# Kernel tuning notes

Hardware: AMD Instinct MI355X
Metric: run time of the kernel (lower is better)

The kernel has to match this reference:

```python
import jax, jax.numpy as jnp
import numpy as np
from jax.scipy.linalg import solve_triangular

EPS = 1e-5
CHUNK = 64

def _rms(x, w, eps=EPS):
    return x * jax.lax.rsqrt(jnp.mean(x * x, axis=-1, keepdims=True) + eps) * w

def _l2norm(x, eps=1e-6):
    return x * jax.lax.rsqrt(jnp.sum(x * x, axis=-1, keepdims=True) + eps)

def _causal_conv(x, w):
    # x: [B,T,C], w: [C,K] depthwise causal short conv
    K = w.shape[1]
    T = x.shape[1]
    xp = jnp.pad(x, ((0, 0), (K - 1, 0), (0, 0)))
    return sum(xp[:, j:j + T, :] * w[:, j] for j in range(K))

def _chunk_gated_delta_rule(q, k, v, g, beta, chunk=CHUNK):
    # q,k: [B,H,T,Dk] (l2-normalized, q pre-scaled); v: [B,H,T,Dv]; g,beta: [B,H,T]
    Bb, H, T, Dk = k.shape
    Dv = v.shape[-1]
    N = T // chunk
    qc, kc, vc = (a.reshape(Bb, H, N, chunk, -1) for a in (q, k, v))
    gc = g.reshape(Bb, H, N, chunk)
    bc = beta.reshape(Bb, H, N, chunk)
    gcs = jnp.cumsum(gc, axis=-1)  # within-chunk cumulative log-decay
    tri = jnp.tril(jnp.ones((chunk, chunk), bool))
    tri_s = jnp.tril(jnp.ones((chunk, chunk), bool), -1)
    diff = gcs[..., :, None] - gcs[..., None, :]
    decay = jnp.where(tri, jnp.exp(jnp.where(tri, diff, 0.0)), 0.0)  # [B,H,N,C,C]
    k_beta = kc * bc[..., None]
    v_beta = vc * bc[..., None]
    A = jnp.einsum('bhnck,bhndk->bhncd', k_beta, kc) * decay
    A = jnp.where(tri_s, A, 0.0)
    eye = jnp.eye(chunk, dtype=q.dtype)
    Tmat = solve_triangular(eye + A, jnp.broadcast_to(eye, A.shape), lower=True)  # (I+A)^-1
    u = Tmat @ v_beta                               # [B,H,N,C,Dv]
    w = Tmat @ (k_beta * jnp.exp(gcs)[..., None])   # [B,H,N,C,Dk]

    def step(S, inp):
        q_i, k_i, u_i, w_i, g_i, dm_i = inp
        attn = jnp.where(tri, jnp.einsum('bhck,bhdk->bhcd', q_i, k_i) * dm_i, 0.0)
        v_new = u_i - w_i @ S
        o_i = (q_i * jnp.exp(g_i)[..., None]) @ S + attn @ v_new
        g_last = g_i[..., -1]
        k_dec = k_i * jnp.exp(g_last[..., None] - g_i)[..., None]
        S = S * jnp.exp(g_last)[..., None, None] + jnp.einsum('bhck,bhcv->bhkv', k_dec, v_new)
        return S, o_i

    xs = tuple(jnp.moveaxis(a, 2, 0) for a in (qc, kc, u, w, gcs, decay))
    S0 = jnp.zeros((Bb, H, Dk, Dv), q.dtype)
    _, outs = jax.lax.scan(step, S0, xs)  # [N,B,H,C,Dv]
    return jnp.moveaxis(outs, 0, 2).reshape(Bb, H, T, Dv)

def _layer_forward(x, mask, ln1_w, qkvz_w, ba_w, conv_w, A_log, dt_bias,
                   o_norm_w, out_w, ln2_w, gate_w, up_w, down_w):
    B, T, D = x.shape
    H = A_log.shape[0]
    kd = qkvz_w.shape[0] // 4  # key_dim == value_dim here (k_heads==v_heads, Dk==Dv)
    vd = kd
    Dk = kd // H
    Dv = vd // H
    silu = jax.nn.silu
    h = _rms(x, ln1_w)
    qkvz = h @ qkvz_w.T
    q, k, v, z = jnp.split(qkvz, [kd, 2 * kd, 2 * kd + vd], axis=-1)
    b, a = jnp.split(h @ ba_w.T, 2, axis=-1)  # [B,T,H] each
    mixed = jnp.concatenate([q, k, v], axis=-1) * mask[..., None]
    mixed = silu(_causal_conv(mixed, conv_w))
    q, k, v = jnp.split(mixed, [kd, 2 * kd], axis=-1)
    q = _l2norm(q.reshape(B, T, H, Dk))
    k = _l2norm(k.reshape(B, T, H, Dk))
    v = v.reshape(B, T, H, Dv)
    beta = jax.nn.sigmoid(b) * mask[..., None]
    g = -jnp.exp(A_log) * jax.nn.softplus(a + dt_bias) * mask[..., None]
    scale = Dk ** -0.5
    bhtd = lambda t: jnp.transpose(t, (0, 2, 1, 3))
    o = _chunk_gated_delta_rule(bhtd(q) * scale, bhtd(k), bhtd(v),
                                jnp.transpose(g, (0, 2, 1)), jnp.transpose(beta, (0, 2, 1)))
    o = jnp.transpose(o, (0, 2, 1, 3))  # [B,T,H,Dv]
    o = _rms(o, o_norm_w) * silu(z.reshape(B, T, H, Dv))  # gated RMSNorm
    x = x + o.reshape(B, T, vd) @ out_w.T
    h2 = _rms(x, ln2_w)
    mlp_out = (silu(h2 @ gate_w.T) * (h2 @ up_w.T)) @ down_w.T
    return x + mlp_out

def setup_inputs():
    key = jax.random.key(0)
    ks = jax.random.split(key, 12)
    B, T, D, H, Dk, Dv, M, K = 1, 4096, 2048, 16, 128, 128, 8192, 4
    kd, vd = H * Dk, H * Dv
    nrm = lambda i, shp, sc=0.02: jax.random.normal(ks[i], shp, jnp.float32) * sc
    return {
        'x': nrm(0, (B, T, D), 1.0),
        'mask': jnp.ones((B, T), jnp.float32),
        'ln1_w': jnp.ones((D,), jnp.float32),
        'qkvz_w': nrm(1, (2 * kd + 2 * vd, D)),
        'ba_w': nrm(2, (2 * H, D)),
        'conv_w': nrm(3, (2 * kd + vd, K), 0.3),
        'A_log': jnp.log(jax.random.uniform(ks[4], (H,), jnp.float32, 1.0, 16.0)),
        'dt_bias': nrm(5, (H,), 0.5),
        'o_norm_w': jnp.ones((Dv,), jnp.float32),
        'out_w': nrm(6, (D, vd)),
        'ln2_w': jnp.ones((D,), jnp.float32),
        'gate_w': nrm(7, (M, D)),
        'up_w': nrm(8, (M, D)),
        'down_w': nrm(9, (D, M)),
    }

def reference(x, mask, ln1_w, qkvz_w, ba_w, conv_w, A_log, dt_bias,
              o_norm_w, out_w, ln2_w, gate_w, up_w, down_w):
    return _layer_forward(x, mask, ln1_w, qkvz_w, ba_w, conv_w, A_log, dt_bias,
                          o_norm_w, out_w, ln2_w, gate_w, up_w, down_w)
```

## Files before the change

kernel.cpp:

```cpp
#include <hip/hip_runtime.h>
#include <math.h>

#define T_LEN 4096
#define DMODEL 2048
#define NH 16
#define CQKV 6144
#define CQKVZ 8192
#define SCALE 0.08838834764831845f

using bf16x8 = __attribute__((ext_vector_type(8))) short;
using f32x4  = __attribute__((ext_vector_type(4))) float;

__device__ __forceinline__ float siluf(float x) { return x / (1.0f + __expf(-x)); }

__device__ __forceinline__ unsigned short f2bf(float f) {
  unsigned int u = __float_as_uint(f);
  u = (u + 0x7FFFu + ((u >> 16) & 1u)) >> 16;
  return (unsigned short)u;
}
__device__ __forceinline__ float bf2f(unsigned short u) {
  return __uint_as_float(((unsigned int)u) << 16);
}
__device__ __forceinline__ ushort4 pack4(float a, float b, float c, float d) {
  ushort4 r; r.x = f2bf(a); r.y = f2bf(b); r.z = f2bf(c); r.w = f2bf(d); return r;
}

__device__ __forceinline__ void gl_lds16(const unsigned short* g, unsigned short* l) {
  __builtin_amdgcn_global_load_lds(
      (const __attribute__((address_space(1))) void*)g,
      (__attribute__((address_space(3))) void*)l, 16, 0, 0);
}

template<int MODE>
__global__ __launch_bounds__(256) void rmsnorm_kernel(const float* __restrict__ x,
                                                      const float* __restrict__ w,
                                                      float* __restrict__ outf,
                                                      unsigned short* __restrict__ outb) {
  const int t = blockIdx.x;
  const int tid = threadIdx.x;
  const float4* xr = (const float4*)(x + (size_t)t * DMODEL);
  float4 v0 = xr[tid];
  float4 v1 = xr[tid + 256];
  float s = v0.x*v0.x + v0.y*v0.y + v0.z*v0.z + v0.w*v0.w
          + v1.x*v1.x + v1.y*v1.y + v1.z*v1.z + v1.w*v1.w;
#pragma unroll
  for (int off = 32; off > 0; off >>= 1) s += __shfl_down(s, off);
  __shared__ float red[4];
  if ((tid & 63) == 0) red[tid >> 6] = s;
  __syncthreads();
  const float tot = red[0] + red[1] + red[2] + red[3];
  const float r = rsqrtf(tot * (1.0f / DMODEL) + 1e-5f);
  const float4* wr = (const float4*)w;
  const float4 w0 = wr[tid], w1 = wr[tid + 256];
  float4 o0, o1;
  o0.x = v0.x*r*w0.x; o0.y = v0.y*r*w0.y; o0.z = v0.z*r*w0.z; o0.w = v0.w*r*w0.w;
  o1.x = v1.x*r*w1.x; o1.y = v1.y*r*w1.y; o1.z = v1.z*r*w1.z; o1.w = v1.w*r*w1.w;
  if (MODE == 1) {
    float4* orow = (float4*)(outf + (size_t)t * DMODEL);
    orow[tid] = o0;
    orow[tid + 256] = o1;
  }
  ushort4* brow = (ushort4*)(outb + (size_t)t * DMODEL);
  brow[tid] = pack4(o0.x, o0.y, o0.z, o0.w);
  brow[tid + 256] = pack4(o1.x, o1.y, o1.z, o1.w);
}

__global__ __launch_bounds__(256) void f2b_kernel(const float* __restrict__ in,
                                                  unsigned short* __restrict__ out) {
  const size_t i = (size_t)blockIdx.x * 256 + threadIdx.x;
  const float4 a = ((const float4*)in)[2 * i];
  const float4 b = ((const float4*)in)[2 * i + 1];
  ((ushort4*)out)[2 * i] = pack4(a.x, a.y, a.z, a.w);
  ((ushort4*)out)[2 * i + 1] = pack4(b.x, b.y, b.z, b.w);
}

template<int EPI, int BM>
__global__ __launch_bounds__(512, 1) void gemm256_kernel(const unsigned short* __restrict__ A,
                                                         const unsigned short* __restrict__ B,
                                                         float* __restrict__ Cf,
                                                         unsigned short* __restrict__ Cb,
                                                         int M, int N, int K) {
  constexpr int BN = 256;
  constexpr int MI = BM / 32;
  constexpr int AW = BM / 128;
  __shared__ __align__(16) unsigned short lds[3][(BM + BN) * 32];
  const int nbm = M / BM, nbn = N / BN, nwg = nbm * nbn;
  const int nt = K >> 5;
  int bmi, bni;
  {
    const int bid = blockIdx.x;
    const int cpx = nwg >> 3;
    int sc = 1;
    while (sc * sc < cpx) sc <<= 1;
    if (sc * sc > cpx) sc >>= 1;
    const int scn = (sc > 0) ? (cpx / sc) : 0;
    if ((nwg & 7) == 0 && sc > 0 && sc * scn == cpx && (nbm % sc) == 0 && (nbn % scn) == 0) {
      const int chunk = bid & 7, widx = bid >> 3;
      const int regc = nbn / scn;
      bmi = (chunk / regc) * sc + widx / scn;
      bni = (chunk % regc) * scn + widx % scn;
    } else {
      bmi = bid / nbn; bni = bid % nbn;
    }
  }
  const int bm = bmi * BM, bn = bni * BN;
  const int tid = threadIdx.x;
  const int wv = tid >> 6, ln = tid & 63;
  const int fr = ln & 15, qq = ln >> 4;
  const int wm = wv >> 2, wn = wv & 3;
  const int ra0 = wm * (BM / 2), rb0 = wn * 64;
  const int lrow = ln >> 2;
  const int lslot = ln & 3;

  f32x4 acc[MI][4];
  const f32x4 zero = {0.f, 0.f, 0.f, 0.f};
#pragma unroll
  for (int mi = 0; mi < MI; mi++)
#pragma unroll
    for (int ni = 0; ni < 4; ni++) acc[mi][ni] = zero;

  auto stageA = [&](int buf, int t) {
    const int k0 = t << 5;
#pragma unroll
    for (int q = 0; q < AW; q++) {
      const int lr = q * 128 + wv * 16 + lrow;
      const int sl = lslot ^ ((lr >> 1) & 3);
      gl_lds16(A + (size_t)(bm + lr) * K + k0 + sl * 8,
               &lds[buf][(q * 128 + wv * 16) * 32]);
    }
  };
  auto stageB = [&](int buf, int t) {
    const int k0 = t << 5;
#pragma unroll
    for (int q = 0; q < 2; q++) {
      const int lr = q * 128 + wv * 16 + lrow;
      const int sl = lslot ^ ((lr >> 1) & 3);
      gl_lds16(B + (size_t)(bn + lr) * K + k0 + sl * 8,
               &lds[buf][BM * 32 + (q * 128 + wv * 16) * 32]);
    }
  };

  stageA(0, 0); stageB(0, 0);
  stageA(1, 1); stageB(1, 1);
  if constexpr (AW == 2) asm volatile("s_waitcnt vmcnt(4)" ::: "memory");
  else                   asm volatile("s_waitcnt vmcnt(3)" ::: "memory");
  __builtin_amdgcn_s_barrier();
  asm volatile("" ::: "memory");

  for (int t = 0; t < nt; t++) {
    const int cb = t % 3;
    const int b2 = (t + 2) % 3;
    const unsigned short* lA = &lds[cb][0];
    const unsigned short* lB = &lds[cb][BM * 32];
    bf16x8 bfr[4];
#pragma unroll
    for (int ni = 0; ni < 4; ni++) {
      const int r = rb0 + ni * 16 + fr;
      bfr[ni] = *(const bf16x8*)&lB[r * 32 + ((qq ^ ((r >> 1) & 3)) << 3)];
    }
    bf16x8 afr[MI];
#pragma unroll
    for (int mi = 0; mi < MI; mi++) {
      const int r = ra0 + mi * 16 + fr;
      afr[mi] = *(const bf16x8*)&lA[r * 32 + ((qq ^ ((r >> 1) & 3)) << 3)];
    }
    if (t + 2 < nt) { stageA(b2, t + 2); stageB(b2, t + 2); }
    __builtin_amdgcn_s_setprio(1);
#pragma unroll
    for (int mi = 0; mi < MI; mi++)
#pragma unroll
      for (int ni = 0; ni < 4; ni++)
        acc[mi][ni] = __builtin_amdgcn_mfma_f32_16x16x32_bf16(afr[mi], bfr[ni], acc[mi][ni], 0, 0, 0);
    __builtin_amdgcn_s_setprio(0);
    if (t + 1 < nt) {
      asm volatile("s_waitcnt lgkmcnt(0)" ::: "memory");
      if (t + 2 < nt) {
        if constexpr (AW == 2) asm volatile("s_waitcnt vmcnt(4)" ::: "memory");
        else                   asm volatile("s_waitcnt vmcnt(3)" ::: "memory");
      } else {
        asm volatile("s_waitcnt vmcnt(0)" ::: "memory");
      }
      __builtin_amdgcn_s_barrier();
      asm volatile("" ::: "memory");
    }
  }

  const int cm4 = qq * 4;
#pragma unroll
  for (int mi = 0; mi < MI; mi++) {
#pragma unroll
    for (int ni = 0; ni < 4; ni++) {
#pragma unroll
      for (int r = 0; r < 4; r++) {
        const int grow = bm + ra0 + mi * 16 + cm4 + r;
        const int gcol = bn + rb0 + ni * 16 + fr;
        const size_t off = (size_t)grow * N + gcol;
        const float v = acc[mi][ni][r];
        if (EPI == 0) {
          Cb[off] = f2bf(v);
        } else if (EPI == 1) {
          Cf[off] += v;
        } else {
          Cb[off] = f2bf(siluf(bf2f(Cb[off])) * v);
        }
      }
    }
  }
}

__global__ __launch_bounds__(256) void ba_gemm_kernel(const float* __restrict__ h_in,
                                                      const float* __restrict__ ba_w,
                                                      float* __restrict__ ba_out) {
  __shared__ __align__(16) float hl[2048];
  __shared__ float red[32][9];
  const int t = blockIdx.x;
  const int tid = threadIdx.x;
  const float4* hr = (const float4*)(h_in + (size_t)t * DMODEL);
  ((float4*)hl)[tid] = hr[tid];
  ((float4*)hl)[tid + 256] = hr[tid + 256];
  __syncthreads();
  const int c = tid & 31;
  const int p = tid >> 5;
  const float* wrow = ba_w + (size_t)c * DMODEL + p * 256;
  const float* hrow = hl + p * 256;
  float s = 0.f;
#pragma unroll 8
  for (int k = 0; k < 256; k++) s += hrow[k] * wrow[k];
  red[c][p] = s;
  __syncthreads();
  if (tid < 32) {
    float tot = 0.f;
#pragma unroll
    for (int q = 0; q < 8; q++) tot += red[tid][q];
    ba_out[(size_t)t * 32 + tid] = tot;
  }
}

__global__ __launch_bounds__(256) void zcopy_kernel(const unsigned short* __restrict__ qkvz,
                                                    unsigned short* __restrict__ z) {
  const int idx = blockIdx.x * 256 + threadIdx.x;
  const int t = idx >> 8;
  const int c8 = (idx & 255) * 8;
  *(uint4*)(z + (size_t)t * 2048 + c8) =
      *(const uint4*)(qkvz + (size_t)t * CQKVZ + CQKV + c8);
}

__global__ __launch_bounds__(256) void conv_silu_kernel(const unsigned short* __restrict__ qkvz,
                                                        const float* __restrict__ conv_w,
                                                        const float* __restrict__ mask,
                                                        float* __restrict__ mixed) {
  const int idx = blockIdx.x * 256 + threadIdx.x;
  const int c4 = (idx % 1536) * 4;
  const int t = idx / 1536;
  const float4 w0 = *(const float4*)(conv_w + (size_t)c4 * 4);
  const float4 w1 = *(const float4*)(conv_w + (size_t)c4 * 4 + 4);
  const float4 w2 = *(const float4*)(conv_w + (size_t)c4 * 4 + 8);
  const float4 w3 = *(const float4*)(conv_w + (size_t)c4 * 4 + 12);
  const float wj0[4] = {w0.x, w0.y, w0.z, w0.w};
  const float wj1[4] = {w1.x, w1.y, w1.z, w1.w};
  const float wj2[4] = {w2.x, w2.y, w2.z, w2.w};
  const float wj3[4] = {w3.x, w3.y, w3.z, w3.w};
  float4 acc = make_float4(0.f, 0.f, 0.f, 0.f);
#pragma unroll
  for (int j = 0; j < 4; j++) {
    const int tt = t - 3 + j;
    if (tt < 0) continue;
    const float m = mask[tt];
    const ushort4 xb = *(const ushort4*)(qkvz + (size_t)tt * CQKVZ + c4);
    acc.x += bf2f(xb.x) * m * wj0[j];
    acc.y += bf2f(xb.y) * m * wj1[j];
    acc.z += bf2f(xb.z) * m * wj2[j];
    acc.w += bf2f(xb.w) * m * wj3[j];
  }
  acc.x = siluf(acc.x); acc.y = siluf(acc.y); acc.z = siluf(acc.z); acc.w = siluf(acc.w);
  *(float4*)(mixed + (size_t)t * CQKV + c4) = acc;
}

__global__ __launch_bounds__(256) void l2norm_kernel(float* __restrict__ mixed) {
  const int r = blockIdx.x * 4 + (threadIdx.x >> 6);
  const int lane = threadIdx.x & 63;
  const int t = r >> 5;
  const int hh = r & 31;
  float* p = mixed + (size_t)t * CQKV + hh * 128 + lane * 2;
  float2 v = *(float2*)p;
  float s = v.x * v.x + v.y * v.y;
#pragma unroll
  for (int off = 32; off > 0; off >>= 1) s += __shfl_down(s, off);
  s = __shfl(s, 0);
  const float rn = rsqrtf(s + 1e-6f);
  v.x *= rn; v.y *= rn;
  *(float2*)p = v;
}

__global__ __launch_bounds__(256) void beta_g_kernel(const float* __restrict__ ba,
                                                     const float* __restrict__ A_log,
                                                     const float* __restrict__ dt_bias,
                                                     const float* __restrict__ mask,
                                                     float* __restrict__ beta,
                                                     float* __restrict__ g) {
  const int idx = blockIdx.x * 256 + threadIdx.x;
  const int t = idx >> 4;
  const int h = idx & 15;
  const float b = ba[(size_t)t * 32 + h];
  const float a = ba[(size_t)t * 32 + 16 + h];
  const float m = mask[t];
  beta[idx] = m / (1.0f + expf(-b));
  const float xx = a + dt_bias[h];
  const float sp = (xx > 20.0f) ? xx : log1pf(expf(xx));
  g[idx] = -expf(A_log[h]) * sp * m;
}

__global__ __launch_bounds__(256) void gcs_kernel(const float* __restrict__ g,
                                                  float* __restrict__ gcsbuf,
                                                  float* __restrict__ edkbuf,
                                                  float* __restrict__ egqbuf,
                                                  float* __restrict__ adecbuf) {
  const int idx = blockIdx.x * 256 + threadIdx.x;
  if (idx >= 1024) return;
  const int h = idx >> 6;
  const int n = idx & 63;
  const int t0 = n * 64;
  float s = 0.f;
  for (int i = 0; i < 64; i++) {
    s += g[(size_t)(t0 + i) * NH + h];
    gcsbuf[(size_t)idx * 64 + i] = s;
  }
  const float glast = s;
  adecbuf[idx] = __expf(glast);
  for (int i = 0; i < 64; i++) {
    const float gi = gcsbuf[(size_t)idx * 64 + i];
    edkbuf[(size_t)idx * 64 + i] = __expf(glast - gi);
    egqbuf[(size_t)idx * 64 + i] = __expf(gi) * SCALE;
  }
}

__global__ __launch_bounds__(256) void pre_attn_kernel(const float* __restrict__ mixed,
                                                       const float* __restrict__ gcsbuf,
                                                       const float* __restrict__ betabuf,
                                                       float* __restrict__ abuf,
                                                       float* __restrict__ attnbuf) {
  __shared__ __align__(16) float kl[64][132];
  __shared__ float gcs_s[64];
  __shared__ float betal[64];
  const int blk = blockIdx.x;
  const int h = blk >> 6;
  const int n = blk & 63;
  const int t0 = n * 64;
  const int tid = threadIdx.x;
  if (tid < 64) {
    gcs_s[tid] = gcsbuf[(size_t)blk * 64 + tid];
    betal[tid] = betabuf[(size_t)(t0 + tid) * NH + h];
  }
#pragma unroll
  for (int rep = 0; rep < 8; rep++) {
    const int lin = rep * 256 + tid;
    const int i = lin >> 5;
    const int d = (lin & 31) * 4;
    const float4 kv = *(const float4*)(mixed + (size_t)(t0 + i) * CQKV + 2048 + h * 128 + d);
    *(float4*)&kl[i][d] = kv;
  }
  __syncthreads();
  const int cj = tid & 15;
  const int ri = tid >> 4;
  const int i0 = ri * 4, j0 = cj * 4;
  float accA[4][4], accQ[4][4];
#pragma unroll
  for (int a = 0; a < 4; a++)
#pragma unroll
    for (int b = 0; b < 4; b++) { accA[a][b] = 0.f; accQ[a][b] = 0.f; }
  const float* qbase = mixed + (size_t)t0 * CQKV + h * 128;
#pragma unroll 4
  for (int d = 0; d < 128; d++) {
    const float kj0 = kl[j0][d], kj1 = kl[j0 + 1][d], kj2 = kl[j0 + 2][d], kj3 = kl[j0 + 3][d];
#pragma unroll
    for (int a = 0; a < 4; a++) {
      const float ka = kl[i0 + a][d];
      const float qa = qbase[(size_t)(i0 + a) * CQKV + d];
      accA[a][0] += ka * kj0; accA[a][1] += ka * kj1; accA[a][2] += ka * kj2; accA[a][3] += ka * kj3;
      accQ[a][0] += qa * kj0; accQ[a][1] += qa * kj1; accQ[a][2] += qa * kj2; accQ[a][3] += qa * kj3;
    }
  }
#pragma unroll
  for (int a = 0; a < 4; a++) {
    const int i = i0 + a;
    const float gi = gcs_s[i];
    const float bi = betal[i];
    float4 Av, Qv;
    float dec;
    dec = __expf(fminf(gi - gcs_s[j0 + 0], 0.f));
    Av.x = (i > j0 + 0) ? accA[a][0] * bi * dec : 0.f;
    Qv.x = (i >= j0 + 0) ? accQ[a][0] * dec * SCALE : 0.f;
    dec = __expf(fminf(gi - gcs_s[j0 + 1], 0.f));
    Av.y = (i > j0 + 1) ? accA[a][1] * bi * dec : 0.f;
    Qv.y = (i >= j0 + 1) ? accQ[a][1] * dec * SCALE : 0.f;
    dec = __expf(fminf(gi - gcs_s[j0 + 2], 0.f));
    Av.z = (i > j0 + 2) ? accA[a][2] * bi * dec : 0.f;
    Qv.z = (i >= j0 + 2) ? accQ[a][2] * dec * SCALE : 0.f;
    dec = __expf(fminf(gi - gcs_s[j0 + 3], 0.f));
    Av.w = (i > j0 + 3) ? accA[a][3] * bi * dec : 0.f;
    Qv.w = (i >= j0 + 3) ? accQ[a][3] * dec * SCALE : 0.f;
    *(float4*)(abuf + (size_t)blk * 4096 + i * 64 + j0) = Av;
    *(float4*)(attnbuf + (size_t)blk * 4096 + i * 64 + j0) = Qv;
  }
}

__global__ __launch_bounds__(256) void pre_solve_kernel(const float* __restrict__ abuf,
                                                        const float* __restrict__ betabuf,
                                                        float* __restrict__ tbuf) {
  __shared__ float Al[64][65];
  __shared__ float Tl[64][65];
  const int blk = blockIdx.x;
  const int h = blk >> 6;
  const int n = blk & 63;
  const int t0 = n * 64;
  const int tid = threadIdx.x;
#pragma unroll
  for (int rep = 0; rep < 4; rep++) {
    const int lin = rep * 256 + tid;
    const int i = lin >> 4;
    const int j = (lin & 15) * 4;
    const float4 av = *(const float4*)(abuf + (size_t)blk * 4096 + i * 64 + j);
    Al[i][j] = av.x; Al[i][j + 1] = av.y; Al[i][j + 2] = av.z; Al[i][j + 3] = av.w;
  }
  __syncthreads();
  if (tid < 64) {
    const int j = tid;
    const float bj = betabuf[(size_t)(t0 + j) * NH + h];
    for (int i = 0; i < 64; i++) {
      float s = (i == j) ? 1.0f : 0.0f;
      for (int l = j; l < i; l++) s -= Al[i][l] * Tl[l][j];
      Tl[i][j] = s;
    }
    for (int i = j; i < 64; i++) Tl[i][j] *= bj;
  }
  __syncthreads();
#pragma unroll
  for (int rep = 0; rep < 4; rep++) {
    const int lin = rep * 256 + tid;
    const int i = lin >> 4;
    const int j = (lin & 15) * 4;
    float4 tv;
    tv.x = Tl[i][j]; tv.y = Tl[i][j + 1]; tv.z = Tl[i][j + 2]; tv.w = Tl[i][j + 3];
    *(float4*)(tbuf + (size_t)blk * 4096 + i * 64 + j) = tv;
  }
}

__global__ __launch_bounds__(256) void pre_uw_kernel(const float* __restrict__ mixed,
                                                     const float* __restrict__ tbuf,
                                                     const float* __restrict__ gcsbuf,
                                                     float* __restrict__ ubuf,
                                                     unsigned short* __restrict__ wbf) {
  __shared__ __align__(16) float Tl[64][68];
  __shared__ __align__(16) float xl[64][132];
  __shared__ float egcs[64];
  const int blk = blockIdx.x;
  const int h = blk >> 6;
  const int n = blk & 63;
  const int t0 = n * 64;
  const int tid = threadIdx.x;
  if (tid < 64) egcs[tid] = __expf(gcsbuf[(size_t)blk * 64 + tid]);
#pragma unroll
  for (int rep = 0; rep < 4; rep++) {
    const int lin = rep * 256 + tid;
    const int i = lin >> 4;
    const int j = (lin & 15) * 4;
    const float4 tv = *(const float4*)(tbuf + (size_t)blk * 4096 + i * 64 + j);
    *(float4*)&Tl[i][j] = tv;
  }
#pragma unroll
  for (int rep = 0; rep < 8; rep++) {
    const int lin = rep * 256 + tid;
    const int i = lin >> 5;
    const int d = (lin & 31) * 4;
    const float4 vv = *(const float4*)(mixed + (size_t)(t0 + i) * CQKV + 4096 + h * 128 + d);
    *(float4*)&xl[i][d] = vv;
  }
  __syncthreads();
  const int cgu = tid & 15;
  const int riu = tid >> 4;
  const int i0 = riu * 4;
  const int d0 = cgu * 8;
  float acc[4][8];
#pragma unroll
  for (int a = 0; a < 4; a++)
#pragma unroll
    for (int b = 0; b < 8; b++) acc[a][b] = 0.f;
#pragma unroll 2
  for (int j = 0; j < 64; j++) {
    const float tv[4] = {Tl[i0][j], Tl[i0 + 1][j], Tl[i0 + 2][j], Tl[i0 + 3][j]};
    const float4 x0 = *(const float4*)&xl[j][d0];
    const float4 x1 = *(const float4*)&xl[j][d0 + 4];
    const float xv[8] = {x0.x, x0.y, x0.z, x0.w, x1.x, x1.y, x1.z, x1.w};
#pragma unroll
    for (int a = 0; a < 4; a++)
#pragma unroll
      for (int b = 0; b < 8; b++) acc[a][b] += tv[a] * xv[b];
  }
#pragma unroll
  for (int a = 0; a < 4; a++) {
    float* up = ubuf + (size_t)(t0 + i0 + a) * 2048 + h * 128 + d0;
    *(float4*)up = make_float4(acc[a][0], acc[a][1], acc[a][2], acc[a][3]);
    *(float4*)(up + 4) = make_float4(acc[a][4], acc[a][5], acc[a][6], acc[a][7]);
  }
  __syncthreads();
#pragma unroll
  for (int rep = 0; rep < 8; rep++) {
    const int lin = rep * 256 + tid;
    const int i = lin >> 5;
    const int d = (lin & 31) * 4;
    float4 kv = *(const float4*)(mixed + (size_t)(t0 + i) * CQKV + 2048 + h * 128 + d);
    const float e = egcs[i];
    kv.x *= e; kv.y *= e; kv.z *= e; kv.w *= e;
    *(float4*)&xl[i][d] = kv;
  }
  __syncthreads();
#pragma unroll
  for (int a = 0; a < 4; a++)
#pragma unroll
    for (int b = 0; b < 8; b++) acc[a][b] = 0.f;
#pragma unroll 2
  for (int j = 0; j < 64; j++) {
    const float tv[4] = {Tl[i0][j], Tl[i0 + 1][j], Tl[i0 + 2][j], Tl[i0 + 3][j]};
    const float4 x0 = *(const float4*)&xl[j][d0];
    const float4 x1 = *(const float4*)&xl[j][d0 + 4];
    const float xv[8] = {x0.x, x0.y, x0.z, x0.w, x1.x, x1.y, x1.z, x1.w};
#pragma unroll
    for (int a = 0; a < 4; a++)
#pragma unroll
      for (int b = 0; b < 8; b++) acc[a][b] += tv[a] * xv[b];
  }
#pragma unroll
  for (int a = 0; a < 4; a++) {
    unsigned short* wp = wbf + (size_t)(t0 + i0 + a) * 2048 + h * 128 + d0;
    *(ushort4*)wp = pack4(acc[a][0], acc[a][1], acc[a][2], acc[a][3]);
    *(ushort4*)(wp + 4) = pack4(acc[a][4], acc[a][5], acc[a][6], acc[a][7]);
  }
}

__global__ __launch_bounds__(256) void ktrans_kernel(const float* __restrict__ mixed,
                                                     const float* __restrict__ edkbuf,
                                                     unsigned short* __restrict__ kdT) {
  __shared__ __align__(16) float kl[64][132];
  __shared__ float edk_s[64];
  const int blk = blockIdx.x;
  const int h = blk >> 6;
  const int n = blk & 63;
  const int t0 = n * 64;
  const int tid = threadIdx.x;
  if (tid < 64) edk_s[tid] = edkbuf[(size_t)blk * 64 + tid];
#pragma unroll
  for (int q = 0; q < 8; q++) {
    const int idx = tid + q * 256;
    const int l = idx >> 5, c4 = (idx & 31) * 4;
    *(float4*)&kl[l][c4] = *(const float4*)(mixed + (size_t)(t0 + l) * CQKV + 2048 + h * 128 + c4);
  }
  __syncthreads();
#pragma unroll
  for (int q = 0; q < 4; q++) {
    const int idx = tid + q * 256;
    const int d = idx >> 3, l8 = (idx & 7) * 8;
    float v[8];
#pragma unroll
    for (int j = 0; j < 8; j++) v[j] = kl[l8 + j][d] * edk_s[l8 + j];
    unsigned short* p = kdT + (size_t)blk * 8192 + d * 64 + l8;
    *(ushort4*)p = pack4(v[0], v[1], v[2], v[3]);
    *(ushort4*)(p + 4) = pack4(v[4], v[5], v[6], v[7]);
  }
}

__global__ __launch_bounds__(512) void scan_kernel(const unsigned short* __restrict__ wbf,
                                                   const unsigned short* __restrict__ kdT,
                                                   const float* __restrict__ ubuf,
                                                   const float* __restrict__ adecbuf,
                                                   unsigned short* __restrict__ STb,
                                                   unsigned short* __restrict__ vtb) {
  __shared__ __align__(16) unsigned short w_lds[64 * 128];
  __shared__ __align__(16) unsigned short kT_lds[128 * 64];
  __shared__ __align__(16) unsigned short st_lds[128 * 128];
  __shared__ __align__(16) unsigned short vt_lds[128 * 64];
  __shared__ __align__(16) float u_lds[64 * 132];
  const int h = blockIdx.x;
  const int tid = threadIdx.x;
  const int ln = tid & 63;
  const int wv = tid >> 6;
  const int fr = ln & 15;
  const int g = ln >> 4;
  const int lt = wv & 3;
  const int ch = wv >> 2;
  const f32x4 zero = {0.f, 0.f, 0.f, 0.f};

  uint4 wreg[2], kreg[2];
  float4 ureg[4];
#pragma unroll
  for (int q = 0; q < 2; q++) {
    const int idx = tid + q * 512;
    const int row = idx >> 4, c8 = (idx & 15) * 8;
    wreg[q] = *(const uint4*)(wbf + (size_t)row * 2048 + h * 128 + c8);
    const int d = idx >> 3, l8 = (idx & 7) * 8;
    kreg[q] = *(const uint4*)(kdT + (size_t)(h * 64) * 8192 + d * 64 + l8);
  }
#pragma unroll
  for (int q = 0; q < 4; q++) {
    const int idx = tid + q * 512;
    const int row = idx >> 5, c4 = (idx & 31) * 4;
    ureg[q] = *(const float4*)(ubuf + (size_t)row * 2048 + h * 128 + c4);
  }

  f32x4 acc2[8];
#pragma unroll
  for (int ct = 0; ct < 8; ct++) acc2[ct] = zero;

  for (int n = 0; n < 64; n++) {
    const int blk = h * 64 + n;
#pragma unroll
    for (int q = 0; q < 2; q++) {
      const int idx = tid + q * 512;
      const int row = idx >> 4, c8 = (idx & 15) * 8;
      *(uint4*)&w_lds[row * 128 + (((c8 >> 3) ^ (row & 7)) << 3)] = wreg[q];
    }
#pragma unroll
    for (int q = 0; q < 4; q++) {
      const int idx = tid + q * 512;
      const int row = idx >> 5, c4 = (idx & 31) * 4;
      *(float4*)&u_lds[row * 132 + c4] = ureg[q];
    }
    {
      const int db = wv * 16 + g * 4;
#pragma unroll
      for (int ct = 0; ct < 8; ct++) {
        const int c = ct * 16 + fr;
        *(ushort4*)&st_lds[c * 128 + (((db >> 3) ^ (c & 7)) << 3) + (db & 7)] =
            pack4(acc2[ct][0], acc2[ct][1], acc2[ct][2], acc2[ct][3]);
      }
    }
    __syncthreads();
#pragma unroll
    for (int q = 0; q < 2; q++) {
      const int idx = tid + q * 512;
      const int d = idx >> 3, l8 = (idx & 7) * 8;
      *(uint4*)&kT_lds[d * 64 + (((l8 >> 3) ^ (d & 7)) << 3)] = kreg[q];
    }
    if (n < 63) {
      const int t0n = (n + 1) * 64;
#pragma unroll
      for (int q = 0; q < 2; q++) {
        const int idx = tid + q * 512;
        const int row = idx >> 4, c8 = (idx & 15) * 8;
        wreg[q] = *(const uint4*)(wbf + (size_t)(t0n + row) * 2048 + h * 128 + c8);
        const int d = idx >> 3, l8 = (idx & 7) * 8;
        kreg[q] = *(const uint4*)(kdT + (size_t)(blk + 1) * 8192 + d * 64 + l8);
      }
#pragma unroll
      for (int q = 0; q < 4; q++) {
        const int idx = tid + q * 512;
        const int row = idx >> 5, c4 = (idx & 31) * 4;
        ureg[q] = *(const float4*)(ubuf + (size_t)(t0n + row) * 2048 + h * 128 + c4);
      }
    }
#pragma unroll
    for (int q = 0; q < 4; q++) {
      const int idx = tid + q * 512;
      const int c = idx >> 4, dg = idx & 15;
      *(uint4*)(STb + (size_t)blk * 16384 + c * 128 + dg * 8) =
          *(const uint4*)&st_lds[c * 128 + ((dg ^ (c & 7)) << 3)];
    }
    f32x4 acc1[4];
#pragma unroll
    for (int ct = 0; ct < 4; ct++) acc1[ct] = zero;
#pragma unroll
    for (int ks = 0; ks < 4; ks++) {
      const int kb = ks * 4 + g;
      const int ar = lt * 16 + fr;
      const bf16x8 a = *(const bf16x8*)&w_lds[ar * 128 + ((kb ^ (ar & 7)) << 3)];
#pragma unroll
      for (int ct = 0; ct < 4; ct++) {
        const int c = (ch * 4 + ct) * 16 + fr;
        const bf16x8 b = *(const bf16x8*)&st_lds[c * 128 + ((kb ^ (c & 7)) << 3)];
        acc1[ct] = __builtin_amdgcn_mfma_f32_16x16x32_bf16(a, b, acc1[ct], 0, 0, 0);
      }
    }
    {
      const int lb = lt * 16 + g * 4;
#pragma unroll
      for (int ct = 0; ct < 4; ct++) {
        const int c = (ch * 4 + ct) * 16 + fr;
        const float v0 = u_lds[(lb + 0) * 132 + c] - acc1[ct][0];
        const float v1 = u_lds[(lb + 1) * 132 + c] - acc1[ct][1];
        const float v2 = u_lds[(lb + 2) * 132 + c] - acc1[ct][2];
        const float v3 = u_lds[(lb + 3) * 132 + c] - acc1[ct][3];
        *(ushort4*)&vt_lds[c * 64 + (((lb >> 3) ^ (c & 7)) << 3) + (lb & 7)] =
            pack4(v0, v1, v2, v3);
      }
    }
    const float adec = adecbuf[blk];
    __syncthreads();
#pragma unroll
    for (int q = 0; q < 2; q++) {
      const int idx = tid + q * 512;
      const int c = idx >> 3, lg = idx & 7;
      *(uint4*)(vtb + (size_t)blk * 8192 + c * 64 + lg * 8) =
          *(const uint4*)&vt_lds[c * 64 + ((lg ^ (c & 7)) << 3)];
    }
#pragma unroll
    for (int ct = 0; ct < 8; ct++) {
      acc2[ct][0] *= adec; acc2[ct][1] *= adec; acc2[ct][2] *= adec; acc2[ct][3] *= adec;
    }
#pragma unroll
    for (int ks = 0; ks < 2; ks++) {
      const int kb = ks * 4 + g;
      const int ar = wv * 16 + fr;
      const bf16x8 a = *(const bf16x8*)&kT_lds[ar * 64 + ((kb ^ (ar & 7)) << 3)];
#pragma unroll
      for (int ct = 0; ct < 8; ct++) {
        const int c = ct * 16 + fr;
        const bf16x8 b = *(const bf16x8*)&vt_lds[c * 64 + ((kb ^ (c & 7)) << 3)];
        acc2[ct] = __builtin_amdgcn_mfma_f32_16x16x32_bf16(a, b, acc2[ct], 0, 0, 0);
      }
    }
  }
}

__global__ __launch_bounds__(256) void ocomp_kernel(const float* __restrict__ mixed,
                                                    const unsigned short* __restrict__ STbuf,
                                                    const unsigned short* __restrict__ vtbuf,
                                                    const float* __restrict__ attnbuf,
                                                    const float* __restrict__ egqbuf,
                                                    const unsigned short* __restrict__ zb,
                                                    const float* __restrict__ onw,
                                                    unsigned short* __restrict__ ob) {
  __shared__ __align__(16) unsigned short STl[128 * 128];
  __shared__ __align__(16) unsigned short vtl[128 * 64];
  __shared__ __align__(16) unsigned short ql[64 * 128];
  __shared__ __align__(16) unsigned short al[64 * 64];
  const int blk = blockIdx.x;
  const int h = blk >> 6;
  const int n = blk & 63;
  const int t0 = n * 64;
  const int tid = threadIdx.x;
#pragma unroll
  for (int q = 0; q < 8; q++) {
    const int idx = tid + q * 256;
    const int c = idx >> 4, dg = idx & 15;
    *(uint4*)&STl[c * 128 + ((dg ^ (c & 7)) << 3)] =
        *(const uint4*)(STbuf + (size_t)blk * 16384 + c * 128 + dg * 8);
  }
#pragma unroll
  for (int q = 0; q < 4; q++) {
    const int idx = tid + q * 256;
    const int c = idx >> 3, lg = idx & 7;
    *(uint4*)&vtl[c * 64 + ((lg ^ (c & 7)) << 3)] =
        *(const uint4*)(vtbuf + (size_t)blk * 8192 + c * 64 + lg * 8);
  }
#pragma unroll
  for (int q = 0; q < 8; q++) {
    const int idx = tid + q * 256;
    const int i = idx >> 5, c4 = (idx & 31) * 4;
    const float eg = egqbuf[(size_t)blk * 64 + i];
    const float4 v = *(const float4*)(mixed + (size_t)(t0 + i) * CQKV + h * 128 + c4);
    *(ushort4*)&ql[i * 128 + (((c4 >> 3) ^ (i & 7)) << 3) + (c4 & 7)] =
        pack4(v.x * eg, v.y * eg, v.z * eg, v.w * eg);
  }
#pragma unroll
  for (int q = 0; q < 4; q++) {
    const int idx = tid + q * 256;
    const int i = idx >> 4, l4 = (idx & 15) * 4;
    const float4 v = *(const float4*)(attnbuf + (size_t)blk * 4096 + i * 64 + l4);
    *(ushort4*)&al[i * 64 + (((l4 >> 3) ^ (i & 7)) << 3) + (l4 & 7)] =
        pack4(v.x, v.y, v.z, v.w);
  }
  __syncthreads();
  const int ln = tid & 63;
  const int wv = tid >> 6;
  const int fr = ln & 15;
  const int g = ln >> 4;
  const int i0 = wv * 16;
  f32x4 acc[8];
  const f32x4 zero = {0.f, 0.f, 0.f, 0.f};
#pragma unroll
  for (int nt = 0; nt < 8; nt++) acc[nt] = zero;
#pragma unroll
  for (int ks = 0; ks < 4; ks++) {
    const int kb = ks * 4 + g;
    const int ar = i0 + fr;
    const bf16x8 a = *(const bf16x8*)&ql[ar * 128 + ((kb ^ (ar & 7)) << 3)];
#pragma unroll
    for (int nt = 0; nt < 8; nt++) {
      const int c = nt * 16 + fr;
      const bf16x8 b = *(const bf16x8*)&STl[c * 128 + ((kb ^ (c & 7)) << 3)];
      acc[nt] = __builtin_amdgcn_mfma_f32_16x16x32_bf16(a, b, acc[nt], 0, 0, 0);
    }
  }
#pragma unroll
  for (int ks = 0; ks < 2; ks++) {
    const int kb = ks * 4 + g;
    const int ar = i0 + fr;
    const bf16x8 a = *(const bf16x8*)&al[ar * 64 + ((kb ^ (ar & 7)) << 3)];
#pragma unroll
    for (int nt = 0; nt < 8; nt++) {
      const int c = nt * 16 + fr;
      const bf16x8 b = *(const bf16x8*)&vtl[c * 64 + ((kb ^ (c & 7)) << 3)];
      acc[nt] = __builtin_amdgcn_mfma_f32_16x16x32_bf16(a, b, acc[nt], 0, 0, 0);
    }
  }
  float s0 = 0.f, s1 = 0.f, s2 = 0.f, s3 = 0.f;
#pragma unroll
  for (int nt = 0; nt < 8; nt++) {
    s0 += acc[nt][0] * acc[nt][0];
    s1 += acc[nt][1] * acc[nt][1];
    s2 += acc[nt][2] * acc[nt][2];
    s3 += acc[nt][3] * acc[nt][3];
  }
#pragma unroll
  for (int m = 1; m < 16; m <<= 1) {
    s0 += __shfl_xor(s0, m);
    s1 += __shfl_xor(s1, m);
    s2 += __shfl_xor(s2, m);
    s3 += __shfl_xor(s3, m);
  }
  float rn[4];
  rn[0] = rsqrtf(s0 * (1.0f / 128.0f) + 1e-5f);
  rn[1] = rsqrtf(s1 * (1.0f / 128.0f) + 1e-5f);
  rn[2] = rsqrtf(s2 * (1.0f / 128.0f) + 1e-5f);
  rn[3] = rsqrtf(s3 * (1.0f / 128.0f) + 1e-5f);
#pragma unroll
  for (int nt = 0; nt < 8; nt++) {
    const int c = nt * 16 + fr;
    const float wn = onw[c];
#pragma unroll
    for (int r = 0; r < 4; r++) {
      const size_t off = (size_t)(t0 + i0 + g * 4 + r) * 2048 + h * 128 + c;
      const float zz = siluf(bf2f(zb[off]));
      ob[off] = f2bf(acc[nt][r] * rn[r] * wn * zz);
    }
  }
}

__global__ __launch_bounds__(256) void copy_kernel(const float* __restrict__ in,
                                                   float* __restrict__ out) {
  const int i = blockIdx.x * 256 + threadIdx.x;
  ((float4*)out)[i] = ((const float4*)in)[i];
}

extern "C" void kernel_launch(void* const* d_in, const int* in_sizes, int n_in,
                              void* d_out, int out_size, void* d_ws, size_t ws_size,
                              hipStream_t stream) {
  (void)in_sizes; (void)n_in; (void)out_size;
  const float* x        = (const float*)d_in[0];
  const float* mask     = (const float*)d_in[1];
  const float* ln1_w    = (const float*)d_in[2];
  const float* qkvz_w   = (const float*)d_in[3];
  const float* ba_w     = (const float*)d_in[4];
  const float* conv_w   = (const float*)d_in[5];
  const float* A_log    = (const float*)d_in[6];
  const float* dt_bias  = (const float*)d_in[7];
  const float* o_norm_w = (const float*)d_in[8];
  const float* out_w    = (const float*)d_in[9];
  const float* ln2_w    = (const float*)d_in[10];
  const float* gate_w   = (const float*)d_in[11];
  const float* up_w     = (const float*)d_in[12];
  const float* down_w   = (const float*)d_in[13];
  float* out = (float*)d_out;

  const size_t NEED_BYTES = (size_t)75825152 * 4;
  if (ws_size < NEED_BYTES) return;

  float* ws = (float*)d_ws;
  float* mixed_buf = ws;
  unsigned short* Wg = (unsigned short*)ws;
  unsigned short* Wu = (unsigned short*)(ws + 8388608);
  unsigned short* Wd = (unsigned short*)(ws + 16777216);
  unsigned short* qkvz_bf = (unsigned short*)(ws + 25165824);
  float* u_buf = ws + 25165824;
  unsigned short* wbf = (unsigned short*)(ws + 33554432);
  unsigned short* kdT = (unsigned short*)(ws + 37748736);
  unsigned short* gate_bf = (unsigned short*)(ws + 25165824);
  unsigned short* z_bf = (unsigned short*)(ws + 41943040);
  float* h_buf = ws + 46137344;
  float* a_buf = ws + 46137344;
  unsigned short* vt_buf = (unsigned short*)(ws + 46137344);
  float* t_buf = ws + 50331648;
  unsigned short* h_bf  = (unsigned short*)(ws + 54525952);
  unsigned short* ob    = (unsigned short*)(ws + 54525952);
  unsigned short* h2_bf = (unsigned short*)(ws + 54525952);
  float* attn_buf = ws + 58720256;
  unsigned short* Wq = (unsigned short*)(ws + 62914560);
  unsigned short* ST_buf = (unsigned short*)(ws + 62914560);
  unsigned short* Wo = (unsigned short*)(ws + 71303168);
  float* ba_buf   = ws + 73400320;
  float* beta_buf = ws + 73531392;
  float* g_buf    = ws + 73596928;
  float* gcs_buf  = ws + 73662464;
  float* edk_buf  = ws + 73728000;
  float* egq_buf  = ws + 73793536;
  float* adec_buf = ws + 73859072;

  rmsnorm_kernel<1><<<4096, 256, 0, stream>>>(x, ln1_w, h_buf, h_bf);
  f2b_kernel<<<8192, 256, 0, stream>>>(qkvz_w, Wq);
  gemm256_kernel<0, 256><<<512, 512, 0, stream>>>(h_bf, Wq, nullptr, qkvz_bf, 4096, 8192, 2048);
  ba_gemm_kernel<<<4096, 256, 0, stream>>>(h_buf, ba_w, ba_buf);
  zcopy_kernel<<<4096, 256, 0, stream>>>(qkvz_bf, z_bf);
  conv_silu_kernel<<<24576, 256, 0, stream>>>(qkvz_bf, conv_w, mask, mixed_buf);
  l2norm_kernel<<<32768, 256, 0, stream>>>(mixed_buf);
  beta_g_kernel<<<256, 256, 0, stream>>>(ba_buf, A_log, dt_bias, mask, beta_buf, g_buf);
  gcs_kernel<<<4, 256, 0, stream>>>(g_buf, gcs_buf, edk_buf, egq_buf, adec_buf);
  pre_attn_kernel<<<1024, 256, 0, stream>>>(mixed_buf, gcs_buf, beta_buf, a_buf, attn_buf);
  pre_solve_kernel<<<1024, 256, 0, stream>>>(a_buf, beta_buf, t_buf);
  pre_uw_kernel<<<1024, 256, 0, stream>>>(mixed_buf, t_buf, gcs_buf, u_buf, wbf);
  ktrans_kernel<<<1024, 256, 0, stream>>>(mixed_buf, edk_buf, kdT);
  scan_kernel<<<16, 512, 0, stream>>>(wbf, kdT, u_buf, adec_buf, ST_buf, vt_buf);
  ocomp_kernel<<<1024, 256, 0, stream>>>(mixed_buf, ST_buf, vt_buf, attn_buf, egq_buf,
                                         z_bf, o_norm_w, ob);
  f2b_kernel<<<8192, 256, 0, stream>>>(gate_w, Wg);
  f2b_kernel<<<8192, 256, 0, stream>>>(up_w, Wu);
  f2b_kernel<<<8192, 256, 0, stream>>>(down_w, Wd);
  f2b_kernel<<<2048, 256, 0, stream>>>(out_w, Wo);
  copy_kernel<<<8192, 256, 0, stream>>>(x, out);
  gemm256_kernel<1, 128><<<256, 512, 0, stream>>>(ob, Wo, out, nullptr, 4096, 2048, 2048);
  rmsnorm_kernel<2><<<4096, 256, 0, stream>>>(out, ln2_w, nullptr, h2_bf);
  gemm256_kernel<0, 256><<<512, 512, 0, stream>>>(h2_bf, Wg, nullptr, gate_bf, 4096, 8192, 2048);
  gemm256_kernel<2, 256><<<512, 512, 0, stream>>>(h2_bf, Wu, nullptr, gate_bf, 4096, 8192, 2048);
  gemm256_kernel<1, 128><<<256, 512, 0, stream>>>(gate_bf, Wd, out, nullptr, 4096, 2048, 8192);
}
```

Measured before the change: 1.480 ms.

## Overlap weight conversions and residual copy with the serial scan kernel

Extra blocks are appended to the 16-block scan launch so they convert the gate, up, down and out weights to bf16 and copy x into the output. This work then runs on otherwise idle CUs while the latency-bound sequential scan executes, and five separate launches go away. The q*exp(g) bf16 pre-scaling moves from ocomp into ktrans, and the scan's __syncthreads calls become manual waitcnt plus s_barrier with sched barriers. The risk is that block scheduling order could delay the 16 scan blocks, and the extra blocks compete with them for memory bandwidth.

```diff
diff --git a/kernel.cpp b/kernel.cpp
--- a/kernel.cpp
+++ b/kernel.cpp
@@ -539,15 +539,21 @@
 
 __global__ __launch_bounds__(256) void ktrans_kernel(const float* __restrict__ mixed,
                                                      const float* __restrict__ edkbuf,
-                                                     unsigned short* __restrict__ kdT) {
+                                                     const float* __restrict__ egqbuf,
+                                                     unsigned short* __restrict__ kdT,
+                                                     unsigned short* __restrict__ qe) {
   __shared__ __align__(16) float kl[64][132];
   __shared__ float edk_s[64];
+  __shared__ float egq_s[64];
   const int blk = blockIdx.x;
   const int h = blk >> 6;
   const int n = blk & 63;
   const int t0 = n * 64;
   const int tid = threadIdx.x;
-  if (tid < 64) edk_s[tid] = edkbuf[(size_t)blk * 64 + tid];
+  if (tid < 64) {
+    edk_s[tid] = edkbuf[(size_t)blk * 64 + tid];
+    egq_s[tid] = egqbuf[(size_t)blk * 64 + tid];
+  }
 #pragma unroll
   for (int q = 0; q < 8; q++) {
     const int idx = tid + q * 256;
@@ -565,6 +571,15 @@
     unsigned short* p = kdT + (size_t)blk * 8192 + d * 64 + l8;
     *(ushort4*)p = pack4(v[0], v[1], v[2], v[3]);
     *(ushort4*)(p + 4) = pack4(v[4], v[5], v[6], v[7]);
+  }
+#pragma unroll
+  for (int q = 0; q < 8; q++) {
+    const int idx = tid + q * 256;
+    const int i = idx >> 5, c4 = (idx & 31) * 4;
+    const float4 v = *(const float4*)(mixed + (size_t)(t0 + i) * CQKV + h * 128 + c4);
+    const float e = egq_s[i];
+    *(ushort4*)(qe + (size_t)(t0 + i) * 2048 + h * 128 + c4) =
+        pack4(v.x * e, v.y * e, v.z * e, v.w * e);
   }
 }
 
@@ -573,12 +588,43 @@
                                                    const float* __restrict__ ubuf,
                                                    const float* __restrict__ adecbuf,
                                                    unsigned short* __restrict__ STb,
-                                                   unsigned short* __restrict__ vtb) {
+                                                   unsigned short* __restrict__ vtb,
+                                                   const float* __restrict__ gw,
+                                                   const float* __restrict__ uw,
+                                                   const float* __restrict__ dw,
+                                                   const float* __restrict__ ow,
+                                                   const float* __restrict__ xin,
+                                                   unsigned short* __restrict__ Wg,
+                                                   unsigned short* __restrict__ Wu,
+                                                   unsigned short* __restrict__ Wd,
+                                                   unsigned short* __restrict__ Wo,
+                                                   float* __restrict__ outc) {
   __shared__ __align__(16) unsigned short w_lds[64 * 128];
   __shared__ __align__(16) unsigned short kT_lds[128 * 64];
   __shared__ __align__(16) unsigned short st_lds[128 * 128];
   __shared__ __align__(16) unsigned short vt_lds[128 * 64];
   __shared__ __align__(16) float u_lds[64 * 132];
+  if (blockIdx.x >= 16) {
+    const int xb = blockIdx.x - 16;
+    const int tid = threadIdx.x;
+    if (xb < 13312) {
+      const float* src;
+      unsigned short* dst;
+      size_t u;
+      if (xb < 4096)       { src = gw; dst = Wg; u = (size_t)xb * 512 + tid; }
+      else if (xb < 8192)  { src = uw; dst = Wu; u = (size_t)(xb - 4096) * 512 + tid; }
+      else if (xb < 12288) { src = dw; dst = Wd; u = (size_t)(xb - 8192) * 512 + tid; }
+      else                 { src = ow; dst = Wo; u = (size_t)(xb - 12288) * 512 + tid; }
+      const float4 a = ((const float4*)src)[2 * u];
+      const float4 b = ((const float4*)src)[2 * u + 1];
+      ((ushort4*)dst)[2 * u] = pack4(a.x, a.y, a.z, a.w);
+      ((ushort4*)dst)[2 * u + 1] = pack4(b.x, b.y, b.z, b.w);
+    } else {
+      const size_t i = (size_t)(xb - 13312) * 512 + tid;
+      ((float4*)outc)[i] = ((const float4*)xin)[i];
+    }
+    return;
+  }
   const int h = blockIdx.x;
   const int tid = threadIdx.x;
   const int ln = tid & 63;
@@ -633,7 +679,10 @@
             pack4(acc2[ct][0], acc2[ct][1], acc2[ct][2], acc2[ct][3]);
       }
     }
-    __syncthreads();
+    asm volatile("s_waitcnt lgkmcnt(0)" ::: "memory");
+    __builtin_amdgcn_sched_barrier(0);
+    asm volatile("s_barrier" ::: "memory");
+    __builtin_amdgcn_sched_barrier(0);
 #pragma unroll
     for (int q = 0; q < 2; q++) {
       const int idx = tid + q * 512;
@@ -693,7 +742,10 @@
       }
     }
     const float adec = adecbuf[blk];
-    __syncthreads();
+    asm volatile("s_waitcnt lgkmcnt(0)" ::: "memory");
+    __builtin_amdgcn_sched_barrier(0);
+    asm volatile("s_barrier" ::: "memory");
+    __builtin_amdgcn_sched_barrier(0);
 #pragma unroll
     for (int q = 0; q < 2; q++) {
       const int idx = tid + q * 512;
@@ -720,11 +772,10 @@
   }
 }
 
-__global__ __launch_bounds__(256) void ocomp_kernel(const float* __restrict__ mixed,
+__global__ __launch_bounds__(256) void ocomp_kernel(const unsigned short* __restrict__ qe,
                                                     const unsigned short* __restrict__ STbuf,
                                                     const unsigned short* __restrict__ vtbuf,
                                                     const float* __restrict__ attnbuf,
-                                                    const float* __restrict__ egqbuf,
                                                     const unsigned short* __restrict__ zb,
                                                     const float* __restrict__ onw,
                                                     unsigned short* __restrict__ ob) {
@@ -752,13 +803,11 @@
         *(const uint4*)(vtbuf + (size_t)blk * 8192 + c * 64 + lg * 8);
   }
 #pragma unroll
-  for (int q = 0; q < 8; q++) {
+  for (int q = 0; q < 4; q++) {
     const int idx = tid + q * 256;
-    const int i = idx >> 5, c4 = (idx & 31) * 4;
-    const float eg = egqbuf[(size_t)blk * 64 + i];
-    const float4 v = *(const float4*)(mixed + (size_t)(t0 + i) * CQKV + h * 128 + c4);
-    *(ushort4*)&ql[i * 128 + (((c4 >> 3) ^ (i & 7)) << 3) + (c4 & 7)] =
-        pack4(v.x * eg, v.y * eg, v.z * eg, v.w * eg);
+    const int i = idx >> 4, dg = idx & 15;
+    *(uint4*)&ql[i * 128 + ((dg ^ (i & 7)) << 3)] =
+        *(const uint4*)(qe + (size_t)(t0 + i) * 2048 + h * 128 + dg * 8);
   }
 #pragma unroll
   for (int q = 0; q < 4; q++) {
@@ -833,12 +882,6 @@
       ob[off] = f2bf(acc[nt][r] * rn[r] * wn * zz);
     }
   }
-}
-
-__global__ __launch_bounds__(256) void copy_kernel(const float* __restrict__ in,
-                                                   float* __restrict__ out) {
-  const int i = blockIdx.x * 256 + threadIdx.x;
-  ((float4*)out)[i] = ((const float4*)in)[i];
 }
 
 extern "C" void kernel_launch(void* const* d_in, const int* in_sizes, int n_in,
@@ -879,6 +922,7 @@
   float* a_buf = ws + 46137344;
   unsigned short* vt_buf = (unsigned short*)(ws + 46137344);
   float* t_buf = ws + 50331648;
+  unsigned short* qe_bf = (unsigned short*)(ws + 50331648);
   unsigned short* h_bf  = (unsigned short*)(ws + 54525952);
   unsigned short* ob    = (unsigned short*)(ws + 54525952);
   unsigned short* h2_bf = (unsigned short*)(ws + 54525952);
@@ -906,15 +950,12 @@
   pre_attn_kernel<<<1024, 256, 0, stream>>>(mixed_buf, gcs_buf, beta_buf, a_buf, attn_buf);
   pre_solve_kernel<<<1024, 256, 0, stream>>>(a_buf, beta_buf, t_buf);
   pre_uw_kernel<<<1024, 256, 0, stream>>>(mixed_buf, t_buf, gcs_buf, u_buf, wbf);
-  ktrans_kernel<<<1024, 256, 0, stream>>>(mixed_buf, edk_buf, kdT);
-  scan_kernel<<<16, 512, 0, stream>>>(wbf, kdT, u_buf, adec_buf, ST_buf, vt_buf);
-  ocomp_kernel<<<1024, 256, 0, stream>>>(mixed_buf, ST_buf, vt_buf, attn_buf, egq_buf,
+  ktrans_kernel<<<1024, 256, 0, stream>>>(mixed_buf, edk_buf, egq_buf, kdT, qe_bf);
+  scan_kernel<<<17424, 512, 0, stream>>>(wbf, kdT, u_buf, adec_buf, ST_buf, vt_buf,
+                                         gate_w, up_w, down_w, out_w, x,
+                                         Wg, Wu, Wd, Wo, out);
+  ocomp_kernel<<<1024, 256, 0, stream>>>(qe_bf, ST_buf, vt_buf, attn_buf,
                                          z_bf, o_norm_w, ob);
-  f2b_kernel<<<8192, 256, 0, stream>>>(gate_w, Wg);
-  f2b_kernel<<<8192, 256, 0, stream>>>(up_w, Wu);
-  f2b_kernel<<<8192, 256, 0, stream>>>(down_w, Wd);
-  f2b_kernel<<<2048, 256, 0, stream>>>(out_w, Wo);
-  copy_kernel<<<8192, 256, 0, stream>>>(x, out);
   gemm256_kernel<1, 128><<<256, 512, 0, stream>>>(ob, Wo, out, nullptr, 4096, 2048, 2048);
   rmsnorm_kernel<2><<<4096, 256, 0, stream>>>(out, ln2_w, nullptr, h2_bf);
   gemm256_kernel<0, 256><<<512, 512, 0, stream>>>(h2_bf, Wg, nullptr, gate_bf, 4096, 8192, 2048);
```

Result: no change. 1.481 ms (+0.1%).
